# Performance work log

Measured on AMD Instinct MI355X. Metric: run time of the kernel, lower is better.

## Reference

```python
import jax, jax.numpy as jnp
import numpy as np

# SAT factor-graph sizes: V variables, F clauses (functions), E edges (3-SAT: E = 3*F)
V = 2000
F = 8400
E = 25200
EPS = 1e-40
MAX_LOGIT = 30.0
PI = 0.0  # pi init kwarg

def safe_log(x):
    return jnp.log(jnp.maximum(x, EPS))

def safe_exp(x):
    return jnp.exp(jnp.minimum(x, MAX_LOGIT))

def setup_inputs() -> dict:
    key = jax.random.key(0)
    ks = jax.random.split(key, 8)
    # each edge connects exactly one variable and one clause
    var_idx = jax.random.randint(ks[0], (E,), 0, V)
    func_idx = jax.random.randint(ks[1], (E,), 0, F)
    edge_feature = (2 * jax.random.randint(ks[2], (E, 1), 0, 2) - 1).astype(jnp.float32)  # +/-1 literal polarity
    variable_mask_T = jax.nn.one_hot(var_idx, V, dtype=jnp.float32)          # [E,V]
    function_mask = jax.nn.one_hot(func_idx, F, dtype=jnp.float32).T        # [F,E]
    p_variable_mask = (variable_mask_T * (edge_feature > 0)).T               # [V,E], positive literals
    n_variable_mask = (variable_mask_T * (edge_feature < 0)).T               # [V,E], negative literals
    # init_state per get_init_state(randomized=True)
    vs = jax.random.uniform(ks[3], (E, 3), dtype=jnp.float32)
    variable_state = vs / vs.sum(1, keepdims=True)
    function_state = jnp.concatenate([jax.random.uniform(ks[4], (E, 1), dtype=jnp.float32), jnp.zeros((E, 1), jnp.float32)], 1)
    dvs = jax.random.uniform(ks[5], (E, 3), dtype=jnp.float32)
    decimator_variable_state = dvs / dvs.sum(1, keepdims=True)
    decimator_function_state = jnp.concatenate([jax.random.uniform(ks[6], (E, 1), dtype=jnp.float32, minval=0.05, maxval=0.95), jnp.zeros((E, 1), jnp.float32)], 1)
    return {
        'variable_state': variable_state,
        'function_state': function_state,
        'decimator_variable_state': decimator_variable_state,
        'decimator_function_state': decimator_function_state,
        'variable_mask_T': variable_mask_T,
        'function_mask': function_mask,
        'p_variable_mask': p_variable_mask,
        'n_variable_mask': n_variable_mask,
        'edge_feature': edge_feature,
    }

def reference(variable_state, function_state, decimator_variable_state, decimator_function_state,
              variable_mask_T, function_mask, p_variable_mask, n_variable_mask, edge_feature):
    # active_mask is None -> mask = ones(E,1); edge_mask is None (decimator_state has length 2)
    mask = jnp.ones((edge_feature.shape[0], 1), dtype=jnp.float32)
    # --- function update: clause-side aggregation of log messages ---
    dvs = safe_log(decimator_variable_state[:, :1])                 # [E,1]
    agg = function_mask.T @ (function_mask @ dvs) - dvs             # sum over clause, minus self
    function_state_new = mask * safe_exp(agg) + (1 - mask) * function_state[:, :1]
    # --- variable update ---
    external_force = decimator_function_state[:, 1:2]               # [E,1]
    dfs = safe_log(1.0 - decimator_function_state[:, :1])           # [E,1]
    pos = variable_mask_T @ (p_variable_mask @ dfs)                 # [E,1]
    neg = variable_mask_T @ (n_variable_mask @ dfs)                 # [E,1]
    ef = edge_feature
    same_sign = 0.5 * (1 + ef) * pos + 0.5 * (1 - ef) * neg - dfs
    same_sign = same_sign + safe_log(1.0 - PI * (external_force == ef).astype(jnp.float32))
    opposite_sign = 0.5 * (1 - ef) * pos + 0.5 * (1 + ef) * neg
    opposite_sign = opposite_sign + safe_log(1.0 - PI * (external_force == -ef).astype(jnp.float32))
    dont_care = safe_exp(same_sign + opposite_sign)
    same_sign = safe_exp(same_sign)
    opposite_sign = safe_exp(opposite_sign)
    q_u = same_sign * (1 - opposite_sign)
    q_s = opposite_sign * (1 - same_sign)
    total = q_u + q_s + dont_care
    temp = jnp.concatenate([q_u, q_s, dont_care], 1) / total        # [E,3]
    variable_state_new = mask * temp + (1 - mask) * variable_state
    return (variable_state_new, jnp.concatenate([function_state_new, external_force], 1))
```

## Files before the change

### kernel.cpp

```cpp
#include <hip/hip_runtime.h>

#define NV 2000
#define NF 8400
#define NE 25200

typedef float f32x4 __attribute__((ext_vector_type(4)));

__device__ __forceinline__ float safe_log(float x) {
    return __logf(fmaxf(x, 1e-40f));
}
__device__ __forceinline__ float safe_exp(float x) {
    return __expf(fminf(x, 30.0f));
}
__device__ __forceinline__ f32x4 ntload(const f32x4* __restrict__ p) {
    return __builtin_nontemporal_load(p);
}

__global__ void k_prep(const float* __restrict__ dec_var,
                       const float* __restrict__ dec_func,
                       float* __restrict__ dvs, float* __restrict__ dfs,
                       float* __restrict__ fsum,
                       float* __restrict__ psum, float* __restrict__ nsum)
{
    unsigned i = blockIdx.x * blockDim.x + threadIdx.x;
    unsigned stride = gridDim.x * blockDim.x;
    for (unsigned e = i; e < NE; e += stride) {
        dvs[e] = safe_log(dec_var[e * 3]);
        dfs[e] = safe_log(1.0f - dec_func[e * 2]);
    }
    for (unsigned f = i; f < NF; f += stride) fsum[f] = 0.0f;
    for (unsigned v = i; v < NV; v += stride) { psum[v] = 0.0f; nsum[v] = 0.0f; }
}


__device__ __forceinline__ void proc_fm(f32x4 x, unsigned i,
                                        const float* __restrict__ dvs,
                                        int* __restrict__ func_idx,
                                        float* __restrict__ fsum)
{
    if (x.x != 0.f || x.y != 0.f || x.z != 0.f || x.w != 0.f) {
        unsigned lin = i * 4u;
        unsigned f = lin / NE;
        unsigned e0 = lin - f * NE;
        float acc = 0.f;
        if (x.x != 0.f) { func_idx[e0 + 0] = (int)f; acc += dvs[e0 + 0]; }
        if (x.y != 0.f) { func_idx[e0 + 1] = (int)f; acc += dvs[e0 + 1]; }
        if (x.z != 0.f) { func_idx[e0 + 2] = (int)f; acc += dvs[e0 + 2]; }
        if (x.w != 0.f) { func_idx[e0 + 3] = (int)f; acc += dvs[e0 + 3]; }
        atomicAdd(&fsum[f], acc);
    }
}

__device__ __forceinline__ void proc_vm(f32x4 x, unsigned i,
                                        const float* __restrict__ dfs,
                                        const float* __restrict__ ef,
                                        int* __restrict__ var_idx,
                                        float* __restrict__ psum,
                                        float* __restrict__ nsum)
{
    if (x.x != 0.f || x.y != 0.f || x.z != 0.f || x.w != 0.f) {
        unsigned lin = i * 4u;
        unsigned e = lin / NV;
        unsigned v = lin - e * NV;
        v += (x.x != 0.f) ? 0u : (x.y != 0.f) ? 1u : (x.z != 0.f) ? 2u : 3u;
        var_idx[e] = (int)v;
        float d = dfs[e];
        if (ef[e] > 0.f) atomicAdd(&psum[v], d);
        else             atomicAdd(&nsum[v], d);
    }
}

#define FM_BLOCKS 2100u
#define VM_BLOCKS 500u
#define SCAN_BLOCKS (FM_BLOCKS + VM_BLOCKS)

__global__ void k_scan(const f32x4* __restrict__ fm, const f32x4* __restrict__ vmT,
                       const float* __restrict__ dvs, const float* __restrict__ dfs,
                       const float* __restrict__ ef,
                       int* __restrict__ func_idx, int* __restrict__ var_idx,
                       float* __restrict__ fsum,
                       float* __restrict__ psum, float* __restrict__ nsum)
{
    if (blockIdx.x < FM_BLOCKS) {
        const unsigned total = NF * NE / 4u;
        const unsigned stride = FM_BLOCKS * 256u;
        unsigned i = blockIdx.x * 256u + threadIdx.x;
        for (; i + 3u * stride < total; i += 4u * stride) {
            f32x4 a = ntload(fm + i);
            f32x4 b = ntload(fm + i + stride);
            f32x4 c = ntload(fm + i + 2u * stride);
            f32x4 d = ntload(fm + i + 3u * stride);
            proc_fm(a, i,               dvs, func_idx, fsum);
            proc_fm(b, i + stride,      dvs, func_idx, fsum);
            proc_fm(c, i + 2u * stride, dvs, func_idx, fsum);
            proc_fm(d, i + 3u * stride, dvs, func_idx, fsum);
        }
        for (; i < total; i += stride)
            proc_fm(ntload(fm + i), i, dvs, func_idx, fsum);
    } else {
        const unsigned total = NE * NV / 4u;
        const unsigned stride = VM_BLOCKS * 256u;
        unsigned i = (blockIdx.x - FM_BLOCKS) * 256u + threadIdx.x;
        for (; i + 3u * stride < total; i += 4u * stride) {
            f32x4 a = ntload(vmT + i);
            f32x4 b = ntload(vmT + i + stride);
            f32x4 c = ntload(vmT + i + 2u * stride);
            f32x4 d = ntload(vmT + i + 3u * stride);
            proc_vm(a, i,               dfs, ef, var_idx, psum, nsum);
            proc_vm(b, i + stride,      dfs, ef, var_idx, psum, nsum);
            proc_vm(c, i + 2u * stride, dfs, ef, var_idx, psum, nsum);
            proc_vm(d, i + 3u * stride, dfs, ef, var_idx, psum, nsum);
        }
        for (; i < total; i += stride)
            proc_vm(ntload(vmT + i), i, dfs, ef, var_idx, psum, nsum);
    }
}

__global__ void k_final(const float* __restrict__ dvs, const float* __restrict__ dfs,
                        const int* __restrict__ var_idx, const int* __restrict__ func_idx,
                        const float* __restrict__ fsum,
                        const float* __restrict__ psum, const float* __restrict__ nsum,
                        const float* __restrict__ ef,
                        const float* __restrict__ dec_func,
                        float* __restrict__ out)
{
    unsigned i = blockIdx.x * blockDim.x + threadIdx.x;
    unsigned stride = gridDim.x * blockDim.x;
    for (unsigned e = i; e < NE; e += stride) {
        float d_vs = dvs[e];
        float d_fs = dfs[e];
        float agg = fsum[func_idx[e]] - d_vs;
        float fstate = safe_exp(agg);
        float extf = dec_func[e * 2 + 1];

        int v = var_idx[e];
        float p = psum[v], n = nsum[v];
        float f = ef[e];
        float ss_log = ((f > 0.f) ? p : n) - d_fs;
        float os_log = ((f > 0.f) ? n : p);
        float dc = safe_exp(ss_log + os_log);
        float ss = safe_exp(ss_log);
        float os = safe_exp(os_log);
        float qu = ss * (1.f - os);
        float qs = os * (1.f - ss);
        float inv = 1.f / (qu + qs + dc);

        out[e * 3 + 0] = qu * inv;
        out[e * 3 + 1] = qs * inv;
        out[e * 3 + 2] = dc * inv;
        out[NE * 3 + e * 2 + 0] = fstate;
        out[NE * 3 + e * 2 + 1] = extf;
    }
}

extern "C" void kernel_launch(void* const* d_in, const int* in_sizes, int n_in,
                              void* d_out, int out_size, void* d_ws, size_t ws_size,
                              hipStream_t stream) {
    const float* dec_var  = (const float*)d_in[2];
    const float* dec_func = (const float*)d_in[3];
    const float* vmT      = (const float*)d_in[4];
    const float* fm       = (const float*)d_in[5];
    const float* ef       = (const float*)d_in[8];
    float* out = (float*)d_out;

    float* ws = (float*)d_ws;
    float* dvs      = ws;
    float* dfs      = ws + NE;
    int*   var_idx  = (int*)(ws + 2 * NE);
    int*   func_idx = (int*)(ws + 3 * NE);
    float* fsum     = ws + 4 * NE;
    float* psum     = fsum + NF;
    float* nsum     = psum + NV;

    k_prep<<<128, 256, 0, stream>>>(dec_var, dec_func, dvs, dfs, fsum, psum, nsum);
    k_scan<<<SCAN_BLOCKS, 256, 0, stream>>>((const f32x4*)fm, (const f32x4*)vmT,
                                            dvs, dfs, ef, func_idx, var_idx,
                                            fsum, psum, nsum);
    k_final<<<128, 256, 0, stream>>>(dvs, dfs, var_idx, func_idx, fsum, psum, nsum,
                                     ef, dec_func, out);
}
```

Baseline: 187.0 us.

## Fold log prep into scan and final kernels, replace prep with memset

Removes the separate prep kernel. The logs of the decimator states are now computed inline, both where the scan consumes them and again in the final kernel, and the accumulators are zeroed with hipMemsetAsync. The scan grid is resized with launch bounds, and the final kernel uses one thread per edge. This saves a kernel launch and the workspace round trip, at the cost of computing the logs twice. The scan is bandwidth-bound on about 1 GB of dense masks, so the overall effect is likely small.

```diff
diff --git a/kernel.cpp b/kernel.cpp
--- a/kernel.cpp
+++ b/kernel.cpp
@@ -16,25 +16,9 @@
     return __builtin_nontemporal_load(p);
 }
 
-__global__ void k_prep(const float* __restrict__ dec_var,
-                       const float* __restrict__ dec_func,
-                       float* __restrict__ dvs, float* __restrict__ dfs,
-                       float* __restrict__ fsum,
-                       float* __restrict__ psum, float* __restrict__ nsum)
-{
-    unsigned i = blockIdx.x * blockDim.x + threadIdx.x;
-    unsigned stride = gridDim.x * blockDim.x;
-    for (unsigned e = i; e < NE; e += stride) {
-        dvs[e] = safe_log(dec_var[e * 3]);
-        dfs[e] = safe_log(1.0f - dec_func[e * 2]);
-    }
-    for (unsigned f = i; f < NF; f += stride) fsum[f] = 0.0f;
-    for (unsigned v = i; v < NV; v += stride) { psum[v] = 0.0f; nsum[v] = 0.0f; }
-}
-
 
 __device__ __forceinline__ void proc_fm(f32x4 x, unsigned i,
-                                        const float* __restrict__ dvs,
+                                        const float* __restrict__ dec_var,
                                         int* __restrict__ func_idx,
                                         float* __restrict__ fsum)
 {
@@ -43,16 +27,16 @@
         unsigned f = lin / NE;
         unsigned e0 = lin - f * NE;
         float acc = 0.f;
-        if (x.x != 0.f) { func_idx[e0 + 0] = (int)f; acc += dvs[e0 + 0]; }
-        if (x.y != 0.f) { func_idx[e0 + 1] = (int)f; acc += dvs[e0 + 1]; }
-        if (x.z != 0.f) { func_idx[e0 + 2] = (int)f; acc += dvs[e0 + 2]; }
-        if (x.w != 0.f) { func_idx[e0 + 3] = (int)f; acc += dvs[e0 + 3]; }
+        if (x.x != 0.f) { func_idx[e0 + 0] = (int)f; acc += safe_log(dec_var[(e0 + 0) * 3]); }
+        if (x.y != 0.f) { func_idx[e0 + 1] = (int)f; acc += safe_log(dec_var[(e0 + 1) * 3]); }
+        if (x.z != 0.f) { func_idx[e0 + 2] = (int)f; acc += safe_log(dec_var[(e0 + 2) * 3]); }
+        if (x.w != 0.f) { func_idx[e0 + 3] = (int)f; acc += safe_log(dec_var[(e0 + 3) * 3]); }
         atomicAdd(&fsum[f], acc);
     }
 }
 
 __device__ __forceinline__ void proc_vm(f32x4 x, unsigned i,
-                                        const float* __restrict__ dfs,
+                                        const float* __restrict__ dec_func,
                                         const float* __restrict__ ef,
                                         int* __restrict__ var_idx,
                                         float* __restrict__ psum,
@@ -64,22 +48,23 @@
         unsigned v = lin - e * NV;
         v += (x.x != 0.f) ? 0u : (x.y != 0.f) ? 1u : (x.z != 0.f) ? 2u : 3u;
         var_idx[e] = (int)v;
-        float d = dfs[e];
+        float d = safe_log(1.0f - dec_func[e * 2]);
         if (ef[e] > 0.f) atomicAdd(&psum[v], d);
         else             atomicAdd(&nsum[v], d);
     }
 }
 
-#define FM_BLOCKS 2100u
-#define VM_BLOCKS 500u
+#define FM_BLOCKS 1654u
+#define VM_BLOCKS 394u
 #define SCAN_BLOCKS (FM_BLOCKS + VM_BLOCKS)
 
-__global__ void k_scan(const f32x4* __restrict__ fm, const f32x4* __restrict__ vmT,
-                       const float* __restrict__ dvs, const float* __restrict__ dfs,
-                       const float* __restrict__ ef,
-                       int* __restrict__ func_idx, int* __restrict__ var_idx,
-                       float* __restrict__ fsum,
-                       float* __restrict__ psum, float* __restrict__ nsum)
+__global__ void __launch_bounds__(256, 8)
+k_scan(const f32x4* __restrict__ fm, const f32x4* __restrict__ vmT,
+       const float* __restrict__ dec_var, const float* __restrict__ dec_func,
+       const float* __restrict__ ef,
+       int* __restrict__ func_idx, int* __restrict__ var_idx,
+       float* __restrict__ fsum,
+       float* __restrict__ psum, float* __restrict__ nsum)
 {
     if (blockIdx.x < FM_BLOCKS) {
         const unsigned total = NF * NE / 4u;
@@ -90,13 +75,13 @@
             f32x4 b = ntload(fm + i + stride);
             f32x4 c = ntload(fm + i + 2u * stride);
             f32x4 d = ntload(fm + i + 3u * stride);
-            proc_fm(a, i,               dvs, func_idx, fsum);
-            proc_fm(b, i + stride,      dvs, func_idx, fsum);
-            proc_fm(c, i + 2u * stride, dvs, func_idx, fsum);
-            proc_fm(d, i + 3u * stride, dvs, func_idx, fsum);
+            proc_fm(a, i,               dec_var, func_idx, fsum);
+            proc_fm(b, i + stride,      dec_var, func_idx, fsum);
+            proc_fm(c, i + 2u * stride, dec_var, func_idx, fsum);
+            proc_fm(d, i + 3u * stride, dec_var, func_idx, fsum);
         }
         for (; i < total; i += stride)
-            proc_fm(ntload(fm + i), i, dvs, func_idx, fsum);
+            proc_fm(ntload(fm + i), i, dec_var, func_idx, fsum);
     } else {
         const unsigned total = NE * NV / 4u;
         const unsigned stride = VM_BLOCKS * 256u;
@@ -106,51 +91,50 @@
             f32x4 b = ntload(vmT + i + stride);
             f32x4 c = ntload(vmT + i + 2u * stride);
             f32x4 d = ntload(vmT + i + 3u * stride);
-            proc_vm(a, i,               dfs, ef, var_idx, psum, nsum);
-            proc_vm(b, i + stride,      dfs, ef, var_idx, psum, nsum);
-            proc_vm(c, i + 2u * stride, dfs, ef, var_idx, psum, nsum);
-            proc_vm(d, i + 3u * stride, dfs, ef, var_idx, psum, nsum);
+            proc_vm(a, i,               dec_func, ef, var_idx, psum, nsum);
+            proc_vm(b, i + stride,      dec_func, ef, var_idx, psum, nsum);
+            proc_vm(c, i + 2u * stride, dec_func, ef, var_idx, psum, nsum);
+            proc_vm(d, i + 3u * stride, dec_func, ef, var_idx, psum, nsum);
         }
         for (; i < total; i += stride)
-            proc_vm(ntload(vmT + i), i, dfs, ef, var_idx, psum, nsum);
+            proc_vm(ntload(vmT + i), i, dec_func, ef, var_idx, psum, nsum);
     }
 }
 
-__global__ void k_final(const float* __restrict__ dvs, const float* __restrict__ dfs,
+__global__ void k_final(const float* __restrict__ dec_var, const float* __restrict__ dec_func,
                         const int* __restrict__ var_idx, const int* __restrict__ func_idx,
                         const float* __restrict__ fsum,
                         const float* __restrict__ psum, const float* __restrict__ nsum,
                         const float* __restrict__ ef,
-                        const float* __restrict__ dec_func,
                         float* __restrict__ out)
 {
-    unsigned i = blockIdx.x * blockDim.x + threadIdx.x;
-    unsigned stride = gridDim.x * blockDim.x;
-    for (unsigned e = i; e < NE; e += stride) {
-        float d_vs = dvs[e];
-        float d_fs = dfs[e];
-        float agg = fsum[func_idx[e]] - d_vs;
-        float fstate = safe_exp(agg);
-        float extf = dec_func[e * 2 + 1];
+    unsigned e = blockIdx.x * blockDim.x + threadIdx.x;
+    if (e >= NE) return;
 
-        int v = var_idx[e];
-        float p = psum[v], n = nsum[v];
-        float f = ef[e];
-        float ss_log = ((f > 0.f) ? p : n) - d_fs;
-        float os_log = ((f > 0.f) ? n : p);
-        float dc = safe_exp(ss_log + os_log);
-        float ss = safe_exp(ss_log);
-        float os = safe_exp(os_log);
-        float qu = ss * (1.f - os);
-        float qs = os * (1.f - ss);
-        float inv = 1.f / (qu + qs + dc);
+    float d_vs = safe_log(dec_var[e * 3]);
+    float d_fs = safe_log(1.0f - dec_func[e * 2]);
+    float extf = dec_func[e * 2 + 1];
 
-        out[e * 3 + 0] = qu * inv;
-        out[e * 3 + 1] = qs * inv;
-        out[e * 3 + 2] = dc * inv;
-        out[NE * 3 + e * 2 + 0] = fstate;
-        out[NE * 3 + e * 2 + 1] = extf;
-    }
+    float agg = fsum[func_idx[e]] - d_vs;
+    float fstate = safe_exp(agg);
+
+    int v = var_idx[e];
+    float p = psum[v], n = nsum[v];
+    float f = ef[e];
+    float ss_log = ((f > 0.f) ? p : n) - d_fs;
+    float os_log = ((f > 0.f) ? n : p);
+    float dc = safe_exp(ss_log + os_log);
+    float ss = safe_exp(ss_log);
+    float os = safe_exp(os_log);
+    float qu = ss * (1.f - os);
+    float qs = os * (1.f - ss);
+    float inv = 1.f / (qu + qs + dc);
+
+    out[e * 3 + 0] = qu * inv;
+    out[e * 3 + 1] = qs * inv;
+    out[e * 3 + 2] = dc * inv;
+    out[NE * 3 + e * 2 + 0] = fstate;
+    out[NE * 3 + e * 2 + 1] = extf;
 }
 
 extern "C" void kernel_launch(void* const* d_in, const int* in_sizes, int n_in,
@@ -164,18 +148,18 @@
     float* out = (float*)d_out;
 
     float* ws = (float*)d_ws;
-    float* dvs      = ws;
-    float* dfs      = ws + NE;
-    int*   var_idx  = (int*)(ws + 2 * NE);
-    int*   func_idx = (int*)(ws + 3 * NE);
-    float* fsum     = ws + 4 * NE;
+    int*   var_idx  = (int*)ws;
+    int*   func_idx = (int*)(ws + NE);
+    float* fsum     = ws + 2 * NE;
     float* psum     = fsum + NF;
     float* nsum     = psum + NV;
 
-    k_prep<<<128, 256, 0, stream>>>(dec_var, dec_func, dvs, dfs, fsum, psum, nsum);
+    hipMemsetAsync(fsum, 0, (NF + 2 * NV) * sizeof(float), stream);
+
     k_scan<<<SCAN_BLOCKS, 256, 0, stream>>>((const f32x4*)fm, (const f32x4*)vmT,
-                                            dvs, dfs, ef, func_idx, var_idx,
-                                            fsum, psum, nsum);
-    k_final<<<128, 256, 0, stream>>>(dvs, dfs, var_idx, func_idx, fsum, psum, nsum,
-                                     ef, dec_func, out);
+                                            dec_var, dec_func, ef,
+                                            func_idx, var_idx, fsum, psum, nsum);
+    k_final<<<(NE + 255) / 256, 256, 0, stream>>>(dec_var, dec_func,
+                                                  var_idx, func_idx,
+                                                  fsum, psum, nsum, ef, out);
 }
```

Result: faster. 182.8 us (-2.3%).
